# Performance work log

Measured on AMD Instinct MI355X. Metric: run time of the kernel, lower is better.

The kernel has to match this reference:

```python
import jax, jax.numpy as jnp
import numpy as np

N = 100000   # nodes
E = 1600000  # edges
F = 128      # node features
H = 64       # hidden_dim
G = 64       # graphs in batch


def setup_inputs() -> dict:
    key = jax.random.key(0)
    ks = jax.random.split(key, 12)
    x = jax.random.normal(ks[0], (N, F), jnp.float32)
    edge_index = jax.random.randint(ks[1], (2, E), 0, N, dtype=jnp.int64)
    batch = jnp.sort(jax.random.randint(ks[2], (N,), 0, G, dtype=jnp.int64))
    s = 0.05
    W1 = jax.random.normal(ks[3], (F, H), jnp.float32) * s
    b1 = jnp.zeros((H,), jnp.float32)
    W2 = jax.random.normal(ks[4], (H, H), jnp.float32) * s
    b2 = jnp.zeros((H,), jnp.float32)
    Wa = jax.random.normal(ks[5], (H, 1), jnp.float32) * s
    ba = jnp.zeros((1,), jnp.float32)
    Wc = jax.random.normal(ks[6], (H, 1), jnp.float32) * s
    bc = jnp.zeros((1,), jnp.float32)
    return {"x": x, "edge_index": edge_index, "batch": batch,
            "W1": W1, "b1": b1, "W2": W2, "b2": b2,
            "Wa": Wa, "ba": ba, "Wc": Wc, "bc": bc}


def _gcn_norm(edge_index, n):
    # Add self-loops, compute symmetric normalization deg^-1/2[src]*deg^-1/2[dst]
    loop = jnp.arange(n, dtype=edge_index.dtype)
    src = jnp.concatenate([edge_index[0], loop])
    dst = jnp.concatenate([edge_index[1], loop])
    deg = jax.ops.segment_sum(jnp.ones_like(src, jnp.float32), dst, num_segments=n)
    dinv = jnp.where(deg > 0, deg ** -0.5, 0.0)
    norm = dinv[src] * dinv[dst]  # [E+N]
    return src, dst, norm


def _gcn_conv(x, W, b, src, dst, norm, n):
    h = x @ W                         # [n, H] dense transform first (PyG order)
    msg = h[src] * norm[:, None]      # gather + normalize [E+n, H]
    agg = jax.ops.segment_sum(msg, dst, num_segments=n)  # scatter-add
    return agg + b


def reference(x, edge_index, batch, W1, b1, W2, b2, Wa, ba, Wc, bc):
    n = x.shape[0]
    src, dst, norm = _gcn_norm(edge_index, n)
    h = jax.nn.relu(_gcn_conv(x, W1, b1, src, dst, norm, n))
    # dropout p=0.1 is identity in eval mode
    h = jax.nn.relu(_gcn_conv(h, W2, b2, src, dst, norm, n))
    action_logits = (h @ Wa + ba)[:, 0]  # [N]
    counts = jax.ops.segment_sum(jnp.ones((n,), jnp.float32), batch, num_segments=G)
    pooled = jax.ops.segment_sum(h, batch, num_segments=G) / jnp.maximum(counts, 1.0)[:, None]
    value = pooled @ Wc + bc  # [G, 1]
    return action_logits, value
```

## Files before the change

### kernel.cpp

```cpp
#include <hip/hip_runtime.h>
#include <hip/hip_fp16.h>
#include <math.h>

#define FEAT 128
#define HID  64
#define BSH  7
#define BNODES (1 << BSH)
#define PB   256
#define SRCM ((1u << 25) - 1)
#define PSPLIT 16


__global__ void part_hist_k(const int* __restrict__ dst, int* __restrict__ table,
                            int e, int nb) {
    __shared__ int lcnt[1024];
    for (int i = threadIdx.x; i < nb; i += 256) lcnt[i] = 0;
    __syncthreads();
    int eb = (e + PB - 1) / PB;
    int lo = blockIdx.x * eb, hi = min(lo + eb, e);
    for (int i = lo + threadIdx.x; i < hi; i += 256)
        atomicAdd(&lcnt[dst[i] >> BSH], 1);
    __syncthreads();
    for (int k = threadIdx.x; k < nb; k += 256)
        table[k * PB + blockIdx.x] = lcnt[k];
}

__global__ void scan1_k(int* __restrict__ data, int* __restrict__ aux, int L) {
    __shared__ int s[1024];
    int gid = blockIdx.x * 1024 + threadIdx.x;
    int v = (gid < L) ? data[gid] : 0;
    s[threadIdx.x] = v;
    __syncthreads();
    for (int off = 1; off < 1024; off <<= 1) {
        int t = (threadIdx.x >= off) ? s[threadIdx.x - off] : 0;
        __syncthreads();
        s[threadIdx.x] += t;
        __syncthreads();
    }
    if (gid < L) data[gid] = s[threadIdx.x] - v;
    if (threadIdx.x == 1023) aux[blockIdx.x] = s[1023];
}

__global__ void scan2_k(int* aux, int naux) {
    __shared__ int s[1024];
    int v = (threadIdx.x < naux) ? aux[threadIdx.x] : 0;
    s[threadIdx.x] = v;
    __syncthreads();
    for (int off = 1; off < 1024; off <<= 1) {
        int t = (threadIdx.x >= off) ? s[threadIdx.x - off] : 0;
        __syncthreads();
        s[threadIdx.x] += t;
        __syncthreads();
    }
    if (threadIdx.x < naux) aux[threadIdx.x] = s[threadIdx.x] - v;
}

__global__ void part_scatter_k(const int* __restrict__ src, const int* __restrict__ dst,
                               const int* __restrict__ table, const int* __restrict__ aux,
                               unsigned* __restrict__ packed, int e, int nb) {
    __shared__ int loff[1024];
    for (int k = threadIdx.x; k < nb; k += 256) {
        int idx = k * PB + blockIdx.x;
        loff[k] = table[idx] + aux[idx >> 10];
    }
    __syncthreads();
    int eb = (e + PB - 1) / PB;
    int lo = blockIdx.x * eb, hi = min(lo + eb, e);
    for (int i = lo + threadIdx.x; i < hi; i += 256) {
        int d = dst[i];
        int p = atomicAdd(&loff[d >> BSH], 1);
        packed[p] = ((unsigned)(d & (BNODES - 1)) << 25) | (unsigned)src[i];
    }
}


__global__ void bucket_sort_k(const unsigned* __restrict__ packed,
                              const int* __restrict__ table, const int* __restrict__ aux,
                              int* __restrict__ col, int* __restrict__ rowptr,
                              float* __restrict__ dinv, int n, int e, int nb) {
    __shared__ int cnt[BNODES];
    __shared__ int s[BNODES];
    __shared__ int cur[BNODES];
    const int k = blockIdx.x;
    const int t = threadIdx.x;
    if (t < BNODES) cnt[t] = 0;
    __syncthreads();
    int i0 = k * PB;
    int i1 = (k + 1) * PB;
    const int bs = table[i0] + aux[i0 >> 10];
    const int be = (k + 1 < nb) ? (table[i1] + aux[i1 >> 10]) : e;
    for (int i = bs + t; i < be; i += 256)
        atomicAdd(&cnt[packed[i] >> 25], 1);
    __syncthreads();
    if (t < BNODES) s[t] = cnt[t];
    __syncthreads();
    for (int off = 1; off < BNODES; off <<= 1) {
        int v = (t < BNODES && t >= off) ? s[t - off] : 0;
        __syncthreads();
        if (t < BNODES) s[t] += v;
        __syncthreads();
    }
    if (t < BNODES) {
        int base = bs + s[t] - cnt[t];
        cur[t] = base;
        int node = (k << BSH) + t;
        if (node < n) {
            rowptr[node] = base;
            dinv[node] = 1.0f / sqrtf(1.0f + (float)cnt[t]);
            if (node == n - 1) rowptr[n] = base + cnt[t];
        }
    }
    __syncthreads();
    for (int i = bs + t; i < be; i += 256) {
        unsigned u = packed[i];
        int p = atomicAdd(&cur[u >> 25], 1);
        col[p] = (int)(u & SRCM);
    }
}


__global__ __launch_bounds__(256, 3)
void gemm_tile_k(const float* __restrict__ X, const float* __restrict__ W,
                 const float* __restrict__ dinv, __half* __restrict__ out, int n) {
    constexpr int K = FEAT;
    __shared__ float sX[64][K + 4];
    __shared__ float sW[64][64];
    const int row0 = blockIdx.x * 64;
    const int t  = threadIdx.x;
    const int tx = t & 15;
    const int ty = t >> 4;

    const float* xb = X + (size_t)row0 * K;
#pragma unroll
    for (int it = 0; it < K / 16; ++it) {
        int fl = it * 1024 + t * 4;
        int r  = fl >> 7;
        int k  = fl & (K - 1);
        float4 v = make_float4(0.f, 0.f, 0.f, 0.f);
        if (row0 + r < n) v = *(const float4*)(xb + fl);
        *(float4*)&sX[r][k] = v;
    }

    float acc[4][4] = {};
#pragma unroll
    for (int ph = 0; ph < K / 64; ++ph) {
        __syncthreads();
#pragma unroll
        for (int it = 0; it < 4; ++it) {
            int fl = it * 1024 + t * 4;
            *(float4*)&sW[fl >> 6][fl & 63] = *(const float4*)(W + ph * 64 * HID + fl);
        }
        __syncthreads();

#pragma unroll 8
        for (int k = 0; k < 64; k += 4) {
            float4 a[4], b[4];
#pragma unroll
            for (int i = 0; i < 4; i++) a[i] = *(float4*)&sX[ty * 4 + i][ph * 64 + k];
#pragma unroll
            for (int j = 0; j < 4; j++) b[j] = *(float4*)&sW[k + j][tx * 4];
#pragma unroll
            for (int i = 0; i < 4; i++) {
                acc[i][0] = fmaf(a[i].x, b[0].x, acc[i][0]);
                acc[i][1] = fmaf(a[i].x, b[0].y, acc[i][1]);
                acc[i][2] = fmaf(a[i].x, b[0].z, acc[i][2]);
                acc[i][3] = fmaf(a[i].x, b[0].w, acc[i][3]);
                acc[i][0] = fmaf(a[i].y, b[1].x, acc[i][0]);
                acc[i][1] = fmaf(a[i].y, b[1].y, acc[i][1]);
                acc[i][2] = fmaf(a[i].y, b[1].z, acc[i][2]);
                acc[i][3] = fmaf(a[i].y, b[1].w, acc[i][3]);
                acc[i][0] = fmaf(a[i].z, b[2].x, acc[i][0]);
                acc[i][1] = fmaf(a[i].z, b[2].y, acc[i][1]);
                acc[i][2] = fmaf(a[i].z, b[2].z, acc[i][2]);
                acc[i][3] = fmaf(a[i].z, b[2].w, acc[i][3]);
                acc[i][0] = fmaf(a[i].w, b[3].x, acc[i][0]);
                acc[i][1] = fmaf(a[i].w, b[3].y, acc[i][1]);
                acc[i][2] = fmaf(a[i].w, b[3].z, acc[i][2]);
                acc[i][3] = fmaf(a[i].w, b[3].w, acc[i][3]);
            }
        }
    }

#pragma unroll
    for (int i = 0; i < 4; i++) {
        int gr = row0 + ty * 4 + i;
        if (gr < n) {
            float sc = dinv[gr];
            union { __half2 h[2]; unsigned long long u; } pk;
            pk.h[0] = __floats2half2_rn(acc[i][0] * sc, acc[i][1] * sc);
            pk.h[1] = __floats2half2_rn(acc[i][2] * sc, acc[i][3] * sc);
            *(unsigned long long*)(out + (size_t)gr * HID + tx * 4) = pk.u;
        }
    }
}


__global__ void gather1_k(const __half* __restrict__ tS, const int* __restrict__ rowptr,
                          const int* __restrict__ col, const float* __restrict__ dinv,
                          const float* __restrict__ b, const float* __restrict__ W2,
                          __half* __restrict__ out, int n) {
    __shared__ __half2 sW2[32][32][2];
    for (int i = threadIdx.x; i < 32 * 32; i += 256) {
        int kk = i >> 5, j = i & 31;
        float2 a = *(const float2*)(W2 + (2 * kk) * HID + 2 * j);
        float2 c = *(const float2*)(W2 + (2 * kk + 1) * HID + 2 * j);
        sW2[kk][j][0] = __floats2half2_rn(a.x, a.y);
        sW2[kk][j][1] = __floats2half2_rn(c.x, c.y);
    }
    __syncthreads();

    int node = (int)((blockIdx.x * (size_t)blockDim.x + threadIdx.x) >> 5);
    int lane = threadIdx.x & 31;
    if (node >= n) return;
    int beg = rowptr[node], end = rowptr[node + 1];
    const __half2* tl = (const __half2*)tS + lane;
    float2 acc = __half22float2(tl[node * 32]);
    int e = beg;
    for (; e + 16 <= end; e += 16) {
        int s[16];
        __half2 v[16];
#pragma unroll
        for (int j = 0; j < 16; j++) s[j] = col[e + j];
#pragma unroll
        for (int j = 0; j < 16; j++) v[j] = tl[s[j] * 32];
        float2 t0 = make_float2(0.f, 0.f), t1 = make_float2(0.f, 0.f);
#pragma unroll
        for (int j = 0; j < 8; j++) {
            float2 f = __half22float2(v[j]);
            t0.x += f.x; t0.y += f.y;
        }
#pragma unroll
        for (int j = 8; j < 16; j++) {
            float2 f = __half22float2(v[j]);
            t1.x += f.x; t1.y += f.y;
        }
        acc.x += t0.x + t1.x;
        acc.y += t0.y + t1.y;
    }
    for (; e + 4 <= end; e += 4) {
        __half2 v0 = tl[col[e] * 32];
        __half2 v1 = tl[col[e + 1] * 32];
        __half2 v2 = tl[col[e + 2] * 32];
        __half2 v3 = tl[col[e + 3] * 32];
        float2 f0 = __half22float2(v0), f1 = __half22float2(v1);
        float2 f2 = __half22float2(v2), f3 = __half22float2(v3);
        acc.x += (f0.x + f1.x) + (f2.x + f3.x);
        acc.y += (f0.y + f1.y) + (f2.y + f3.y);
    }
    for (; e < end; ++e) {
        float2 f = __half22float2(tl[col[e] * 32]);
        acc.x += f.x; acc.y += f.y;
    }
    float d = dinv[node];
    float2 bb = *(const float2*)(b + 2 * lane);
    float h0 = fmaxf(fmaf(d, acc.x, bb.x), 0.0f);
    float h1 = fmaxf(fmaf(d, acc.y, bb.y), 0.0f);

    __half2 hh = __floats2half2_rn(h0, h1);
    int hu = *(int*)&hh;
    float2 o = make_float2(0.f, 0.f);
#pragma unroll
    for (int kk = 0; kk < 32; ++kk) {
        int pu = __shfl(hu, kk, 32);
        __half2 hv = *(__half2*)&pu;
        float2 hf = __half22float2(hv);
        float2 w0 = __half22float2(sW2[kk][lane][0]);
        float2 w1 = __half22float2(sW2[kk][lane][1]);
        o.x = fmaf(hf.x, w0.x, o.x); o.y = fmaf(hf.x, w0.y, o.y);
        o.x = fmaf(hf.y, w1.x, o.x); o.y = fmaf(hf.y, w1.y, o.y);
    }
    ((__half2*)out)[node * 32 + lane] = __floats2half2_rn(o.x * d, o.y * d);
}


__global__ void gather2_k(const __half* __restrict__ tS, const int* __restrict__ rowptr,
                          const int* __restrict__ col, const float* __restrict__ dinv,
                          const float* __restrict__ b, __half* __restrict__ out,
                          const float* __restrict__ Wa, const float* __restrict__ ba,
                          float* __restrict__ logits, int n) {
    int node = (int)((blockIdx.x * (size_t)blockDim.x + threadIdx.x) >> 5);
    int lane = threadIdx.x & 31;
    if (node >= n) return;
    int beg = rowptr[node], end = rowptr[node + 1];
    const __half2* tl = (const __half2*)tS + lane;
    float2 acc = __half22float2(tl[node * 32]);
    int e = beg;
    for (; e + 16 <= end; e += 16) {
        int s[16];
        __half2 v[16];
#pragma unroll
        for (int j = 0; j < 16; j++) s[j] = col[e + j];
#pragma unroll
        for (int j = 0; j < 16; j++) v[j] = tl[s[j] * 32];
        float2 t0 = make_float2(0.f, 0.f), t1 = make_float2(0.f, 0.f);
#pragma unroll
        for (int j = 0; j < 8; j++) {
            float2 f = __half22float2(v[j]);
            t0.x += f.x; t0.y += f.y;
        }
#pragma unroll
        for (int j = 8; j < 16; j++) {
            float2 f = __half22float2(v[j]);
            t1.x += f.x; t1.y += f.y;
        }
        acc.x += t0.x + t1.x;
        acc.y += t0.y + t1.y;
    }
    for (; e + 4 <= end; e += 4) {
        __half2 v0 = tl[col[e] * 32];
        __half2 v1 = tl[col[e + 1] * 32];
        __half2 v2 = tl[col[e + 2] * 32];
        __half2 v3 = tl[col[e + 3] * 32];
        float2 f0 = __half22float2(v0), f1 = __half22float2(v1);
        float2 f2 = __half22float2(v2), f3 = __half22float2(v3);
        acc.x += (f0.x + f1.x) + (f2.x + f3.x);
        acc.y += (f0.y + f1.y) + (f2.y + f3.y);
    }
    for (; e < end; ++e) {
        float2 f = __half22float2(tl[col[e] * 32]);
        acc.x += f.x; acc.y += f.y;
    }
    float d = dinv[node];
    float2 bb = *(const float2*)(b + 2 * lane);
    float h0 = fmaxf(fmaf(d, acc.x, bb.x), 0.0f);
    float h1 = fmaxf(fmaf(d, acc.y, bb.y), 0.0f);
    ((__half2*)out)[node * 32 + lane] = __floats2half2_rn(h0, h1);
    float2 wa = *(const float2*)(Wa + 2 * lane);
    float p = h0 * wa.x + h1 * wa.y;
#pragma unroll
    for (int off = 16; off > 0; off >>= 1) p += __shfl_down(p, off, 32);
    if (lane == 0) logits[node] = p + ba[0];
}


__global__ void pool2_k(const __half* __restrict__ h, const int* __restrict__ batch,
                        float* __restrict__ pooled, int n) {
    const int gid  = blockIdx.x / PSPLIT;
    const int part = blockIdx.x % PSPLIT;
    int lo = 0, hi = n;
    while (lo < hi) { int m = (lo + hi) >> 1; if (batch[m] < gid) lo = m + 1; else hi = m; }
    const int b0 = lo;
    hi = n;
    while (lo < hi) { int m = (lo + hi) >> 1; if (batch[m] < gid + 1) lo = m + 1; else hi = m; }
    const int b1 = lo;
    const int chunk = (b1 - b0 + PSPLIT - 1) / PSPLIT;
    const int r0 = b0 + part * chunk;
    const int r1 = min(r0 + chunk, b1);
    const int lane = threadIdx.x & 31;
    const int rg   = threadIdx.x >> 5;
    const __half2* hp = (const __half2*)h + lane;
    float2 acc = make_float2(0.f, 0.f);
    for (int i = r0 + rg; i < r1; i += 8) {
        float2 f = __half22float2(hp[(size_t)i * 32]);
        acc.x += f.x; acc.y += f.y;
    }
    __shared__ float2 red[8][32];
    red[rg][lane] = acc;
    __syncthreads();
    if (threadIdx.x < 32) {
        float2 s = make_float2(0.f, 0.f);
#pragma unroll
        for (int r = 0; r < 8; r++) { s.x += red[r][threadIdx.x].x; s.y += red[r][threadIdx.x].y; }
        atomicAdd(&pooled[gid * HID + 2 * threadIdx.x], s.x);
        atomicAdd(&pooled[gid * HID + 2 * threadIdx.x + 1], s.y);
    }
}


__global__ void value_k(const float* __restrict__ pooled, const int* __restrict__ batch,
                        const float* __restrict__ Wc, const float* __restrict__ bc,
                        float* __restrict__ val, int n, int g) {
    int gw   = (int)((blockIdx.x * (size_t)blockDim.x + threadIdx.x) >> 6);
    int lane = threadIdx.x & 63;
    if (gw >= g) return;
    int lo = 0, hi = n;
    while (lo < hi) { int m = (lo + hi) >> 1; if (batch[m] < gw) lo = m + 1; else hi = m; }
    int b0 = lo;
    lo = 0; hi = n;
    while (lo < hi) { int m = (lo + hi) >> 1; if (batch[m] < gw + 1) lo = m + 1; else hi = m; }
    float cnt = fmaxf((float)(lo - b0), 1.0f);
    float p = (pooled[gw * HID + lane] / cnt) * Wc[lane];
#pragma unroll
    for (int off = 32; off > 0; off >>= 1) p += __shfl_down(p, off);
    if (lane == 0) val[gw] = p + bc[0];
}

extern "C" void kernel_launch(void* const* d_in, const int* in_sizes, int n_in,
                              void* d_out, int out_size, void* d_ws, size_t ws_size,
                              hipStream_t stream) {
    const float* x     = (const float*)d_in[0];
    const int*   ei    = (const int*)d_in[1];
    const int*   batch = (const int*)d_in[2];
    const float* W1    = (const float*)d_in[3];
    const float* b1    = (const float*)d_in[4];
    const float* W2    = (const float*)d_in[5];
    const float* b2    = (const float*)d_in[6];
    const float* Wa    = (const float*)d_in[7];
    const float* ba    = (const float*)d_in[8];
    const float* Wc    = (const float*)d_in[9];
    const float* bc    = (const float*)d_in[10];

    const int n = in_sizes[0] / FEAT;
    const int e = in_sizes[1] / 2;
    const int g = out_size - n;
    const int* src = ei;
    const int* dst = ei + e;

    const int nb = (n + BNODES - 1) >> BSH;
    const int L  = nb * PB;

    float*    ws     = (float*)d_ws;
    float*    dinv   = ws;
    float*    bufA   = dinv + n;
    float*    bufB   = bufA + (size_t)n * HID;
    float*    pooled = bufB + (size_t)n * HID;
    int*      table  = (int*)(pooled + (size_t)g * HID);
    int*      aux    = table + L;
    int*      rowptr = aux + 1024;
    int*      col    = rowptr + n + 1;
    unsigned* packed = (unsigned*)bufA;
    __half*   tS1    = (__half*)bufA;
    __half*   tS2    = (__half*)bufB;
    __half*   h2     = (__half*)bufA;

    const int B = 256;
    const int gridT = (n + 63) / 64;
    const int gridG = (int)(((size_t)n * 32 + B - 1) / B);
    const int nb1   = (L + 1023) / 1024;

    (void)hipMemsetAsync(pooled, 0, (size_t)g * HID * sizeof(float), stream);

    part_hist_k<<<PB, B, 0, stream>>>(dst, table, e, nb);
    scan1_k<<<nb1, 1024, 0, stream>>>(table, aux, L);
    scan2_k<<<1, 1024, 0, stream>>>(aux, nb1);
    part_scatter_k<<<PB, B, 0, stream>>>(src, dst, table, aux, packed, e, nb);
    bucket_sort_k<<<nb, B, 0, stream>>>(packed, table, aux, col, rowptr, dinv, n, e, nb);

    gemm_tile_k<<<gridT, B, 0, stream>>>(x, W1, dinv, tS1, n);
    gather1_k<<<gridG, B, 0, stream>>>(tS1, rowptr, col, dinv, b1, W2, tS2, n);

    gather2_k<<<gridG, B, 0, stream>>>(tS2, rowptr, col, dinv, b2, h2,
                                       Wa, ba, (float*)d_out, n);

    pool2_k<<<g * PSPLIT, B, 0, stream>>>(h2, batch, pooled, n);
    value_k<<<(g * 64 + B - 1) / B, B, 0, stream>>>(pooled, batch, Wc, bc,
                                                    (float*)d_out + n, n, g);
}
```

Before: 304.8 us.

## Split layer-2 transform out of gather into separate MFMA GEMM kernel

Removes the per-node 64x64 shuffle-based matvec fused into gather1_k and writes the relu'd hidden features to a buffer instead. A new kernel, t2_k, multiplies them by W2 with 16x16x32 f16 MFMA instructions, one 16-row strip per wave, and scales each row by dinv. The goal is to replace a long chain of shuffles and scalar FMAs in the gather with matrix-core work. In exchange it adds a launch and an extra round trip of an N×64 half buffer through memory.

Measured after the change: 296.6 us. 1.03x faster.

```diff
diff --git a/kernel.cpp b/kernel.cpp
--- a/kernel.cpp
+++ b/kernel.cpp
@@ -9,6 +9,10 @@
 #define PB   256
 #define SRCM ((1u << 25) - 1)
 #define PSPLIT 16
+
+typedef _Float16 f16_t;
+typedef f16_t half8 __attribute__((ext_vector_type(8)));
+typedef float  f32x4 __attribute__((ext_vector_type(4)));
 
 
 __global__ void part_hist_k(const int* __restrict__ dst, int* __restrict__ table,
@@ -197,18 +201,7 @@
 
 __global__ void gather1_k(const __half* __restrict__ tS, const int* __restrict__ rowptr,
                           const int* __restrict__ col, const float* __restrict__ dinv,
-                          const float* __restrict__ b, const float* __restrict__ W2,
-                          __half* __restrict__ out, int n) {
-    __shared__ __half2 sW2[32][32][2];
-    for (int i = threadIdx.x; i < 32 * 32; i += 256) {
-        int kk = i >> 5, j = i & 31;
-        float2 a = *(const float2*)(W2 + (2 * kk) * HID + 2 * j);
-        float2 c = *(const float2*)(W2 + (2 * kk + 1) * HID + 2 * j);
-        sW2[kk][j][0] = __floats2half2_rn(a.x, a.y);
-        sW2[kk][j][1] = __floats2half2_rn(c.x, c.y);
-    }
-    __syncthreads();
-
+                          const float* __restrict__ b, __half* __restrict__ out, int n) {
     int node = (int)((blockIdx.x * (size_t)blockDim.x + threadIdx.x) >> 5);
     int lane = threadIdx.x & 31;
     if (node >= n) return;
@@ -255,21 +248,53 @@
     float2 bb = *(const float2*)(b + 2 * lane);
     float h0 = fmaxf(fmaf(d, acc.x, bb.x), 0.0f);
     float h1 = fmaxf(fmaf(d, acc.y, bb.y), 0.0f);
-
-    __half2 hh = __floats2half2_rn(h0, h1);
-    int hu = *(int*)&hh;
-    float2 o = make_float2(0.f, 0.f);
-#pragma unroll
-    for (int kk = 0; kk < 32; ++kk) {
-        int pu = __shfl(hu, kk, 32);
-        __half2 hv = *(__half2*)&pu;
-        float2 hf = __half22float2(hv);
-        float2 w0 = __half22float2(sW2[kk][lane][0]);
-        float2 w1 = __half22float2(sW2[kk][lane][1]);
-        o.x = fmaf(hf.x, w0.x, o.x); o.y = fmaf(hf.x, w0.y, o.y);
-        o.x = fmaf(hf.y, w1.x, o.x); o.y = fmaf(hf.y, w1.y, o.y);
-    }
-    ((__half2*)out)[node * 32 + lane] = __floats2half2_rn(o.x * d, o.y * d);
+    ((__half2*)out)[node * 32 + lane] = __floats2half2_rn(h0, h1);
+}
+
+
+__global__ __launch_bounds__(256)
+void t2_k(const __half* __restrict__ h, const float* __restrict__ W2,
+          const float* __restrict__ dinv, __half* __restrict__ out, int n) {
+    const int wave  = threadIdx.x >> 6;
+    const int l     = threadIdx.x & 63;
+    const int strip = blockIdx.x * 4 + wave;
+    const int r0    = strip * 16;
+    if (r0 >= n) return;
+    const int col = l & 15;
+    const int kb  = l >> 4;
+
+    half8 bf[4][2];
+#pragma unroll
+    for (int t = 0; t < 4; ++t)
+#pragma unroll
+        for (int kk = 0; kk < 2; ++kk)
+#pragma unroll
+            for (int j = 0; j < 8; ++j)
+                bf[t][kk][j] = (f16_t)W2[(kk * 32 + kb * 8 + j) * HID + t * 16 + col];
+
+    const int arow = r0 + col;
+    const __half* ap = h + (size_t)arow * HID + kb * 8;
+    half8 a0 = *(const half8*)(ap);
+    half8 a1 = *(const half8*)(ap + 32);
+
+    f32x4 acc[4] = {};
+#pragma unroll
+    for (int t = 0; t < 4; ++t) {
+        acc[t] = __builtin_amdgcn_mfma_f32_16x16x32_f16(a0, bf[t][0], acc[t], 0, 0, 0);
+        acc[t] = __builtin_amdgcn_mfma_f32_16x16x32_f16(a1, bf[t][1], acc[t], 0, 0, 0);
+    }
+
+    const int rbase = r0 + kb * 4;
+#pragma unroll
+    for (int r = 0; r < 4; ++r) {
+        int gr = rbase + r;
+        if (gr < n) {
+            float dv = dinv[gr];
+#pragma unroll
+            for (int t = 0; t < 4; ++t)
+                out[(size_t)gr * HID + t * 16 + col] = __float2half(acc[t][r] * dv);
+        }
+    }
 }
 
 
@@ -420,13 +445,16 @@
     int*      col    = rowptr + n + 1;
     unsigned* packed = (unsigned*)bufA;
     __half*   tS1    = (__half*)bufA;
-    __half*   tS2    = (__half*)bufB;
-    __half*   h2     = (__half*)bufA;
+    __half*   h16    = (__half*)bufB;
+    __half*   tS2    = (__half*)bufA;
+    __half*   h2     = (__half*)bufB;
 
     const int B = 256;
-    const int gridT = (n + 63) / 64;
-    const int gridG = (int)(((size_t)n * 32 + B - 1) / B);
-    const int nb1   = (L + 1023) / 1024;
+    const int gridT  = (n + 63) / 64;
+    const int gridG  = (int)(((size_t)n * 32 + B - 1) / B);
+    const int strips = (n + 15) / 16;
+    const int gridT2 = (strips + 3) / 4;
+    const int nb1    = (L + 1023) / 1024;
 
     (void)hipMemsetAsync(pooled, 0, (size_t)g * HID * sizeof(float), stream);
 
@@ -437,8 +465,9 @@
     bucket_sort_k<<<nb, B, 0, stream>>>(packed, table, aux, col, rowptr, dinv, n, e, nb);
 
     gemm_tile_k<<<gridT, B, 0, stream>>>(x, W1, dinv, tS1, n);
-    gather1_k<<<gridG, B, 0, stream>>>(tS1, rowptr, col, dinv, b1, W2, tS2, n);
-
+    gather1_k<<<gridG, B, 0, stream>>>(tS1, rowptr, col, dinv, b1, h16, n);
+
+    t2_k<<<gridT2, B, 0, stream>>>(h16, W2, dinv, tS2, n);
     gather2_k<<<gridG, B, 0, stream>>>(tS2, rowptr, col, dinv, b2, h2,
                                        Wa, ba, (float*)d_out, n);
 
```

## Use MFMA for fused layer-2 transform and fold pooling, value and memset

Applied to the files above, without the earlier changes.

The fused layer-1 aggregation plus W2 transform now runs on 16-node blocks of 512 threads. After a shared-memory staging step, 4 waves compute the 16x64 product with the 16x16x32 f16 MFMA instruction, replacing the per-lane shuffle-based FMA loop. The pooled memset moves into the first histogram kernel, and the value head is folded into the pooling kernel through a last-block ticket counter. Together these cut launches and the scalar matmul cost, in exchange for W2 being reloaded from global memory in every block and a threadfence/atomic ticket at the end of pooling.

Result: slower. 463.9 us (+52.2%).

```diff
diff --git a/kernel.cpp b/kernel.cpp
--- a/kernel.cpp
+++ b/kernel.cpp
@@ -10,9 +10,18 @@
 #define SRCM ((1u << 25) - 1)
 #define PSPLIT 16
 
+typedef _Float16 f16_t;
+typedef f16_t half8 __attribute__((ext_vector_type(8)));
+typedef float  f32x4 __attribute__((ext_vector_type(4)));
+
 
 __global__ void part_hist_k(const int* __restrict__ dst, int* __restrict__ table,
-                            int e, int nb) {
+                            float* __restrict__ pooled, int* __restrict__ ticket,
+                            int e, int nb, int gh) {
+    if (blockIdx.x == 0) {
+        for (int i = threadIdx.x; i < gh; i += 256) pooled[i] = 0.0f;
+        if (threadIdx.x == 0) ticket[0] = 0;
+    }
     __shared__ int lcnt[1024];
     for (int i = threadIdx.x; i < nb; i += 256) lcnt[i] = 0;
     __syncthreads();
@@ -195,81 +204,95 @@
 }
 
 
-__global__ void gather1_k(const __half* __restrict__ tS, const int* __restrict__ rowptr,
-                          const int* __restrict__ col, const float* __restrict__ dinv,
-                          const float* __restrict__ b, const float* __restrict__ W2,
-                          __half* __restrict__ out, int n) {
-    __shared__ __half2 sW2[32][32][2];
-    for (int i = threadIdx.x; i < 32 * 32; i += 256) {
-        int kk = i >> 5, j = i & 31;
-        float2 a = *(const float2*)(W2 + (2 * kk) * HID + 2 * j);
-        float2 c = *(const float2*)(W2 + (2 * kk + 1) * HID + 2 * j);
-        sW2[kk][j][0] = __floats2half2_rn(a.x, a.y);
-        sW2[kk][j][1] = __floats2half2_rn(c.x, c.y);
-    }
-    __syncthreads();
-
-    int node = (int)((blockIdx.x * (size_t)blockDim.x + threadIdx.x) >> 5);
-    int lane = threadIdx.x & 31;
-    if (node >= n) return;
-    int beg = rowptr[node], end = rowptr[node + 1];
-    const __half2* tl = (const __half2*)tS + lane;
-    float2 acc = __half22float2(tl[node * 32]);
-    int e = beg;
-    for (; e + 16 <= end; e += 16) {
-        int s[16];
-        __half2 v[16];
-#pragma unroll
-        for (int j = 0; j < 16; j++) s[j] = col[e + j];
-#pragma unroll
-        for (int j = 0; j < 16; j++) v[j] = tl[s[j] * 32];
-        float2 t0 = make_float2(0.f, 0.f), t1 = make_float2(0.f, 0.f);
-#pragma unroll
-        for (int j = 0; j < 8; j++) {
-            float2 f = __half22float2(v[j]);
-            t0.x += f.x; t0.y += f.y;
-        }
-#pragma unroll
-        for (int j = 8; j < 16; j++) {
-            float2 f = __half22float2(v[j]);
-            t1.x += f.x; t1.y += f.y;
-        }
-        acc.x += t0.x + t1.x;
-        acc.y += t0.y + t1.y;
-    }
-    for (; e + 4 <= end; e += 4) {
-        __half2 v0 = tl[col[e] * 32];
-        __half2 v1 = tl[col[e + 1] * 32];
-        __half2 v2 = tl[col[e + 2] * 32];
-        __half2 v3 = tl[col[e + 3] * 32];
-        float2 f0 = __half22float2(v0), f1 = __half22float2(v1);
-        float2 f2 = __half22float2(v2), f3 = __half22float2(v3);
-        acc.x += (f0.x + f1.x) + (f2.x + f3.x);
-        acc.y += (f0.y + f1.y) + (f2.y + f3.y);
-    }
-    for (; e < end; ++e) {
-        float2 f = __half22float2(tl[col[e] * 32]);
-        acc.x += f.x; acc.y += f.y;
-    }
-    float d = dinv[node];
-    float2 bb = *(const float2*)(b + 2 * lane);
-    float h0 = fmaxf(fmaf(d, acc.x, bb.x), 0.0f);
-    float h1 = fmaxf(fmaf(d, acc.y, bb.y), 0.0f);
-
-    __half2 hh = __floats2half2_rn(h0, h1);
-    int hu = *(int*)&hh;
-    float2 o = make_float2(0.f, 0.f);
-#pragma unroll
-    for (int kk = 0; kk < 32; ++kk) {
-        int pu = __shfl(hu, kk, 32);
-        __half2 hv = *(__half2*)&pu;
-        float2 hf = __half22float2(hv);
-        float2 w0 = __half22float2(sW2[kk][lane][0]);
-        float2 w1 = __half22float2(sW2[kk][lane][1]);
-        o.x = fmaf(hf.x, w0.x, o.x); o.y = fmaf(hf.x, w0.y, o.y);
-        o.x = fmaf(hf.y, w1.x, o.x); o.y = fmaf(hf.y, w1.y, o.y);
-    }
-    ((__half2*)out)[node * 32 + lane] = __floats2half2_rn(o.x * d, o.y * d);
+__global__ __launch_bounds__(512)
+void gather1t2_k(const __half* __restrict__ tS, const int* __restrict__ rowptr,
+                 const int* __restrict__ col, const float* __restrict__ dinv,
+                 const float* __restrict__ b, const float* __restrict__ W2,
+                 __half* __restrict__ out, int n) {
+    __shared__ __half sh[16][72];
+    const int tid  = threadIdx.x;
+    const int nl   = tid >> 5;
+    const int lane = tid & 31;
+    const int r0   = blockIdx.x * 16;
+    const int node = r0 + nl;
+
+    float h0 = 0.f, h1 = 0.f;
+    if (node < n) {
+        int beg = rowptr[node], end = rowptr[node + 1];
+        const __half2* tl = (const __half2*)tS + lane;
+        float2 acc = __half22float2(tl[node * 32]);
+        int e = beg;
+        for (; e + 16 <= end; e += 16) {
+            int s[16];
+            __half2 v[16];
+#pragma unroll
+            for (int j = 0; j < 16; j++) s[j] = col[e + j];
+#pragma unroll
+            for (int j = 0; j < 16; j++) v[j] = tl[s[j] * 32];
+            float2 t0 = make_float2(0.f, 0.f), t1 = make_float2(0.f, 0.f);
+#pragma unroll
+            for (int j = 0; j < 8; j++) {
+                float2 f = __half22float2(v[j]);
+                t0.x += f.x; t0.y += f.y;
+            }
+#pragma unroll
+            for (int j = 8; j < 16; j++) {
+                float2 f = __half22float2(v[j]);
+                t1.x += f.x; t1.y += f.y;
+            }
+            acc.x += t0.x + t1.x;
+            acc.y += t0.y + t1.y;
+        }
+        for (; e + 4 <= end; e += 4) {
+            __half2 v0 = tl[col[e] * 32];
+            __half2 v1 = tl[col[e + 1] * 32];
+            __half2 v2 = tl[col[e + 2] * 32];
+            __half2 v3 = tl[col[e + 3] * 32];
+            float2 f0 = __half22float2(v0), f1 = __half22float2(v1);
+            float2 f2 = __half22float2(v2), f3 = __half22float2(v3);
+            acc.x += (f0.x + f1.x) + (f2.x + f3.x);
+            acc.y += (f0.y + f1.y) + (f2.y + f3.y);
+        }
+        for (; e < end; ++e) {
+            float2 f = __half22float2(tl[col[e] * 32]);
+            acc.x += f.x; acc.y += f.y;
+        }
+        float d = dinv[node];
+        float2 bb = *(const float2*)(b + 2 * lane);
+        h0 = fmaxf(fmaf(d, acc.x, bb.x), 0.0f);
+        h1 = fmaxf(fmaf(d, acc.y, bb.y), 0.0f);
+    }
+    *(__half2*)&sh[nl][2 * lane] = __floats2half2_rn(h0, h1);
+    __syncthreads();
+
+    const int w = tid >> 6;
+    if (w < 4) {
+        const int l    = tid & 63;
+        const int colc = l & 15;
+        const int kb   = l >> 4;
+        const int t    = w;
+        half8 b0, b1;
+#pragma unroll
+        for (int j = 0; j < 8; ++j)
+            b0[j] = (f16_t)W2[(kb * 8 + j) * HID + t * 16 + colc];
+#pragma unroll
+        for (int j = 0; j < 8; ++j)
+            b1[j] = (f16_t)W2[(32 + kb * 8 + j) * HID + t * 16 + colc];
+        half8 a0 = *(const half8*)&sh[colc][kb * 8];
+        half8 a1 = *(const half8*)&sh[colc][32 + kb * 8];
+        f32x4 acc = {};
+        acc = __builtin_amdgcn_mfma_f32_16x16x32_f16(a0, b0, acc, 0, 0, 0);
+        acc = __builtin_amdgcn_mfma_f32_16x16x32_f16(a1, b1, acc, 0, 0, 0);
+        const int rbase = r0 + kb * 4;
+#pragma unroll
+        for (int r = 0; r < 4; ++r) {
+            int gr = rbase + r;
+            if (gr < n) {
+                float dv = dinv[gr];
+                out[(size_t)gr * HID + t * 16 + colc] = __float2half(acc[r] * dv);
+            }
+        }
+    }
 }
 
 
@@ -333,8 +356,10 @@
 }
 
 
-__global__ void pool2_k(const __half* __restrict__ h, const int* __restrict__ batch,
-                        float* __restrict__ pooled, int n) {
+__global__ void poolvalue_k(const __half* __restrict__ h, const int* __restrict__ batch,
+                            float* __restrict__ pooled, int* __restrict__ ticket,
+                            const float* __restrict__ Wc, const float* __restrict__ bc,
+                            float* __restrict__ val, int n, int g) {
     const int gid  = blockIdx.x / PSPLIT;
     const int part = blockIdx.x % PSPLIT;
     int lo = 0, hi = n;
@@ -364,25 +389,27 @@
         atomicAdd(&pooled[gid * HID + 2 * threadIdx.x], s.x);
         atomicAdd(&pooled[gid * HID + 2 * threadIdx.x + 1], s.y);
     }
-}
-
-
-__global__ void value_k(const float* __restrict__ pooled, const int* __restrict__ batch,
-                        const float* __restrict__ Wc, const float* __restrict__ bc,
-                        float* __restrict__ val, int n, int g) {
-    int gw   = (int)((blockIdx.x * (size_t)blockDim.x + threadIdx.x) >> 6);
-    int lane = threadIdx.x & 63;
-    if (gw >= g) return;
-    int lo = 0, hi = n;
-    while (lo < hi) { int m = (lo + hi) >> 1; if (batch[m] < gw) lo = m + 1; else hi = m; }
-    int b0 = lo;
-    lo = 0; hi = n;
-    while (lo < hi) { int m = (lo + hi) >> 1; if (batch[m] < gw + 1) lo = m + 1; else hi = m; }
-    float cnt = fmaxf((float)(lo - b0), 1.0f);
-    float p = (pooled[gw * HID + lane] / cnt) * Wc[lane];
-#pragma unroll
-    for (int off = 32; off > 0; off >>= 1) p += __shfl_down(p, off);
-    if (lane == 0) val[gw] = p + bc[0];
+
+    __threadfence();
+    __shared__ int tk;
+    if (threadIdx.x == 0) tk = atomicAdd(ticket, 1);
+    __syncthreads();
+    if (tk == g * PSPLIT - 1) {
+        const int lane64 = threadIdx.x & 63;
+        const int wv     = threadIdx.x >> 6;
+        for (int gw = wv; gw < g; gw += 4) {
+            int l2 = 0, h2 = n;
+            while (l2 < h2) { int m = (l2 + h2) >> 1; if (batch[m] < gw) l2 = m + 1; else h2 = m; }
+            int s0 = l2;
+            h2 = n;
+            while (l2 < h2) { int m = (l2 + h2) >> 1; if (batch[m] < gw + 1) l2 = m + 1; else h2 = m; }
+            float cnt = fmaxf((float)(l2 - s0), 1.0f);
+            float p = (pooled[gw * HID + lane64] / cnt) * Wc[lane64];
+#pragma unroll
+            for (int off = 32; off > 0; off >>= 1) p += __shfl_down(p, off);
+            if (lane64 == 0) val[gw] = p + bc[0];
+        }
+    }
 }
 
 extern "C" void kernel_launch(void* const* d_in, const int* in_sizes, int n_in,
@@ -414,7 +441,8 @@
     float*    bufA   = dinv + n;
     float*    bufB   = bufA + (size_t)n * HID;
     float*    pooled = bufB + (size_t)n * HID;
-    int*      table  = (int*)(pooled + (size_t)g * HID);
+    int*      ticket = (int*)(pooled + (size_t)g * HID);
+    int*      table  = ticket + 1;
     int*      aux    = table + L;
     int*      rowptr = aux + 1024;
     int*      col    = rowptr + n + 1;
@@ -424,25 +452,23 @@
     __half*   h2     = (__half*)bufA;
 
     const int B = 256;
-    const int gridT = (n + 63) / 64;
-    const int gridG = (int)(((size_t)n * 32 + B - 1) / B);
-    const int nb1   = (L + 1023) / 1024;
-
-    (void)hipMemsetAsync(pooled, 0, (size_t)g * HID * sizeof(float), stream);
-
-    part_hist_k<<<PB, B, 0, stream>>>(dst, table, e, nb);
+    const int gridT  = (n + 63) / 64;
+    const int gridG  = (int)(((size_t)n * 32 + B - 1) / B);
+    const int gridF  = (n + 15) / 16;
+    const int nb1    = (L + 1023) / 1024;
+
+    part_hist_k<<<PB, B, 0, stream>>>(dst, table, pooled, ticket, e, nb, g * HID);
     scan1_k<<<nb1, 1024, 0, stream>>>(table, aux, L);
     scan2_k<<<1, 1024, 0, stream>>>(aux, nb1);
     part_scatter_k<<<PB, B, 0, stream>>>(src, dst, table, aux, packed, e, nb);
     bucket_sort_k<<<nb, B, 0, stream>>>(packed, table, aux, col, rowptr, dinv, n, e, nb);
 
     gemm_tile_k<<<gridT, B, 0, stream>>>(x, W1, dinv, tS1, n);
-    gather1_k<<<gridG, B, 0, stream>>>(tS1, rowptr, col, dinv, b1, W2, tS2, n);
+    gather1t2_k<<<gridF, 512, 0, stream>>>(tS1, rowptr, col, dinv, b1, W2, tS2, n);
 
     gather2_k<<<gridG, B, 0, stream>>>(tS2, rowptr, col, dinv, b2, h2,
                                        Wa, ba, (float*)d_out, n);
 
-    pool2_k<<<g * PSPLIT, B, 0, stream>>>(h2, batch, pooled, n);
-    value_k<<<(g * 64 + B - 1) / B, B, 0, stream>>>(pooled, batch, Wc, bc,
-                                                    (float*)d_out + n, n, g);
-}
+    poolvalue_k<<<g * PSPLIT, B, 0, stream>>>(h2, batch, pooled, ticket, Wc, bc,
+                                              (float*)d_out + n, n, g);
+}
```
